# Performance work log

Hardware: AMD Instinct MI355X
Metric: run time of the kernel (lower is better)

Reference implementation:

```python
import jax, jax.numpy as jnp
import numpy as np

L, B, S, D, N, H = 4, 4, 1024, 1024, 64, 16   # layers, batch, seq, d_model, d_state, heads
DI = 2 * D      # d_inner (expand_factor=2)
DH = D // H     # head dim
DF = 4 * D      # ffn hidden
SCALE = 1.0 / np.sqrt(DH)


def setup_inputs() -> dict:
    key = jax.random.key(0)
    ks = jax.random.split(key, 12)
    w = lambda k, sh: jax.random.normal(k, sh, jnp.float32) * 0.02
    return {
        "x": jax.random.normal(ks[0], (B, S, D), jnp.float32),
        "A_log": jax.random.normal(ks[1], (L, N), jnp.float32),
        "Dp": jax.random.normal(ks[2], (L, D), jnp.float32),
        "W_in": w(ks[3], (L, 2 * DI, D)), "b_in": jnp.zeros((L, 2 * DI), jnp.float32),
        "W_xp": w(ks[4], (L, N, DI)), "b_xp": jnp.zeros((L, N), jnp.float32),
        "W_dt": w(ks[5], (L, D, DI)), "b_dt": jnp.zeros((L, D), jnp.float32),
        "W_out": w(ks[6], (L, D, DI)), "b_out": jnp.zeros((L, D), jnp.float32),
        "W_qkv": w(ks[7], (L, 3 * D, D)), "b_qkv": jnp.zeros((L, 3 * D), jnp.float32),
        "W_ao": w(ks[8], (L, D, D)), "b_ao": jnp.zeros((L, D), jnp.float32),
        "g1": jnp.ones((L, D), jnp.float32), "be1": jnp.zeros((L, D), jnp.float32),
        "g2": jnp.ones((L, D), jnp.float32), "be2": jnp.zeros((L, D), jnp.float32),
        "W_f1": w(ks[9], (L, DF, D)), "b_f1": jnp.zeros((L, DF), jnp.float32),
        "W_f2": w(ks[10], (L, D, DF)), "b_f2": jnp.zeros((L, D), jnp.float32),
    }


def _ln(x, g, b, eps=1e-5):
    mu = x.mean(-1, keepdims=True)
    var = ((x - mu) ** 2).mean(-1, keepdims=True)
    return (x - mu) * jax.lax.rsqrt(var + eps) * g + b


def _mamba(x, A_log, Dp, W_in, b_in, W_xp, b_xp, W_dt, b_dt, W_out, b_out):
    xr = jnp.einsum('bsd,od->bso', x, W_in) + b_in          # [b,s,2*DI]
    xi, res = jnp.split(xr, 2, axis=-1)
    xi = jax.nn.silu(xi)
    A = -jnp.exp(A_log)                                      # [N]
    delta = jax.nn.softplus(jnp.einsum('bsi,di->bsd', xi, W_dt) + b_dt)  # [b,s,D]
    m = delta.mean(-1)                                       # [b,s]
    A_disc = jnp.exp(A[None, None, :] * m[:, :, None])       # [b,s,N]
    u = jnp.einsum('bsi,ni->bsn', xi, W_xp) + b_xp           # [b,s,N]

    def step(state, inp):
        a_t, u_t = inp
        state = a_t * state + u_t                            # [b,N]
        return state, state.sum(-1)                          # carry, emit sum over d_state

    init = jnp.zeros((x.shape[0], A_log.shape[0]), x.dtype)
    _, ssum = jax.lax.scan(step, init, (A_disc.swapaxes(0, 1), u.swapaxes(0, 1)))
    ssum = ssum.swapaxes(0, 1)                               # [b,s]
    y = ssum[..., None] * xi                                 # [b,s,DI]
    y = y * jax.nn.silu(res)
    y = jnp.einsum('bsi,di->bsd', y, W_out) + b_out
    return y + x * Dp


def _attn(x, W_qkv, b_qkv, W_ao, b_ao):
    b, s, d = x.shape
    qkv = jnp.einsum('bsd,od->bso', x, W_qkv) + b_qkv        # [b,s,3d]
    qkv = qkv.reshape(b, s, 3, H, DH)
    q = jnp.moveaxis(qkv[:, :, 0], 2, 1)                     # [b,h,s,dh]
    k = jnp.moveaxis(qkv[:, :, 1], 2, 1)
    v = jnp.moveaxis(qkv[:, :, 2], 2, 1)
    scores = jnp.einsum('bhqd,bhkd->bhqk', q, k) * SCALE
    wts = jax.nn.softmax(scores, axis=-1)
    o = jnp.einsum('bhqk,bhkd->bhqd', wts, v)
    o = jnp.moveaxis(o, 1, 2).reshape(b, s, d)
    return jnp.einsum('bsd,od->bso', o, W_ao) + b_ao


def _forward(x, A_log, Dp, W_in, b_in, W_xp, b_xp, W_dt, b_dt, W_out, b_out,
             W_qkv, b_qkv, W_ao, b_ao, g1, be1, g2, be2, W_f1, b_f1, W_f2, b_f2):
    for l in range(L):
        m = _mamba(x, A_log[l], Dp[l], W_in[l], b_in[l], W_xp[l], b_xp[l],
                   W_dt[l], b_dt[l], W_out[l], b_out[l])
        x = _ln(x + m, g1[l], be1[l])
        a = _attn(x, W_qkv[l], b_qkv[l], W_ao[l], b_ao[l])
        x = _ln(x + a, g2[l], be2[l])
        h = jax.nn.gelu(jnp.einsum('bsd,fd->bsf', x, W_f1[l]) + b_f1[l], approximate=False)
        x = x + jnp.einsum('bsf,df->bsd', h, W_f2[l]) + b_f2[l]
    return x


def reference(x, A_log, Dp, W_in, b_in, W_xp, b_xp, W_dt, b_dt, W_out, b_out,
              W_qkv, b_qkv, W_ao, b_ao, g1, be1, g2, be2, W_f1, b_f1, W_f2, b_f2):
    return _forward(x, A_log, Dp, W_in, b_in, W_xp, b_xp, W_dt, b_dt, W_out, b_out,
                    W_qkv, b_qkv, W_ao, b_ao, g1, be1, g2, be2, W_f1, b_f1, W_f2, b_f2)
```

## Files before the change

kernel.cpp:

```cpp
#include <hip/hip_runtime.h>
#include <math.h>

typedef unsigned short ushort_t;
typedef unsigned int uint_t;
typedef __attribute__((ext_vector_type(8))) short short8;
typedef __attribute__((ext_vector_type(4))) float f32x4;

constexpr int Bb = 4, Ss = 1024, Dd = 1024, Nn = 64, Hh = 16;
constexpr int DIi = 2048, DFf = 4096;
constexpr int TOKENS = Bb * Ss;

constexpr size_t O_IN  = 0;
constexpr size_t O_DT  = 4194304;
constexpr size_t O_XP  = O_DT + 2097152;
constexpr size_t O_OUT = O_XP + 262144;
constexpr size_t O_QKV = O_OUT + 2097152;
constexpr size_t O_AO  = O_QKV + 3145728;
constexpr size_t O_F1  = O_AO + 1048576;
constexpr size_t O_F2  = O_F1 + 4194304;
constexpr size_t W_TOTAL = O_F2 + 4194304;
constexpr size_t W_QUADS = W_TOTAL / 4;

enum { EPI_SPLIT = 0, EPI_QKV, EPI_GELU, EPI_DTXP, EPI_DP, EPI_F32, EPI_RESID };

__device__ __forceinline__ float siluf(float x) { return x / (1.f + expf(-x)); }
__device__ __forceinline__ float softplusf(float x) { return fmaxf(x, 0.f) + log1pf(expf(-fabsf(x))); }
__device__ __forceinline__ float geluf(float x) { return 0.5f * x * (1.f + erff(x * 0.7071067811865476f)); }

__device__ __forceinline__ float bf2f(uint_t u) {
    union { uint_t i; float f; } v; v.i = u << 16; return v.f;
}
__device__ __forceinline__ ushort_t f2bf(float f) {
    union { float f; uint_t i; } v; v.f = f;
    return (ushort_t)((v.i + 0x7FFFu + ((v.i >> 16) & 1u)) >> 16);
}

__device__ __forceinline__ void gload_lds16(const ushort_t* g, ushort_t* l) {
    __builtin_amdgcn_global_load_lds(
        (const __attribute__((address_space(1))) unsigned int*)g,
        (__attribute__((address_space(3))) unsigned int*)l, 16, 0, 0);
}

__device__ __forceinline__ void wait_vm(int n) {
    if (n == 0)      asm volatile("s_waitcnt vmcnt(0)" ::: "memory");
    else if (n == 3) asm volatile("s_waitcnt vmcnt(3)" ::: "memory");
    else if (n == 4) asm volatile("s_waitcnt vmcnt(4)" ::: "memory");
    else if (n == 6) asm volatile("s_waitcnt vmcnt(6)" ::: "memory");
    else             asm volatile("s_waitcnt vmcnt(8)" ::: "memory");
}

template <int EPI, int MT, int NBUF, int XBY>
__global__ __launch_bounds__(256) void gemm_mfma(
    const ushort_t* __restrict__ A, const ushort_t* __restrict__ Bw,
    const float* __restrict__ bias, int M, int N, int K,
    float* __restrict__ of0, float* __restrict__ of1,
    ushort_t* __restrict__ ob0, ushort_t* __restrict__ ob1,
    const float* __restrict__ e0, const float* __restrict__ e1)
{
    constexpr int BUFSZ = (MT == 128) ? 8192 : 6144;
    constexpr int DEPTH = NBUF - 1;
    constexpr int L     = (MT == 128) ? 4 : 3;
    constexpr int NJ    = (MT == 128) ? 4 : 2;
    constexpr int XBX   = 8 / XBY;
    __shared__ __attribute__((aligned(16))) ushort_t AB[NBUF * BUFSZ];

    const int tid = threadIdx.x;
    const int lane = tid & 63, wid = tid >> 6;
    const int wr = (MT == 128) ? (wid >> 1) : 0;
    const int wc = (MT == 128) ? (wid & 1) : wid;
    const int l15 = lane & 15, lg = lane >> 4;

    int bx = blockIdx.x, by = blockIdx.y;
    const int gx = gridDim.x, gy = gridDim.y;
    if ((gy % XBY) == 0 && (gx % XBX) == 0) {
        const int s = by * gx + bx;
        const int xcd = s & 7, c = s >> 3;
        const int gyc = gy / XBY, gxc = gx / XBX;
        by = (xcd % XBY) * gyc + (c % gyc);
        bx = (xcd / XBY) * gxc + (c / gyc);
    }
    const int m0 = by * MT, n0 = bx << 7;

    f32x4 acc[4][NJ];
#pragma unroll
    for (int i = 0; i < 4; ++i)
#pragma unroll
        for (int j = 0; j < NJ; ++j) { acc[i][j][0] = 0.f; acc[i][j][1] = 0.f; acc[i][j][2] = 0.f; acc[i][j][3] = 0.f; }

    const int srow4 = lane >> 2;
    const int scc4  = (lane & 3) ^ ((lane >> 3) & 3);
    const ushort_t* Ag = A + (size_t)(m0 + wid * 32 + srow4) * K + scc4 * 8;
    const ushort_t* Bg = Bw + (size_t)(n0 + wid * 32 + srow4) * K + scc4 * 8;
    const ushort_t* sb64[3];
    int do64[3];
    if (MT == 64) {
#pragma unroll
        for (int j = 0; j < 3; ++j) {
            const int i = wid * 3 + j;
            const bool isA = i < 4;
            const int rb = (isA ? i : i - 4) * 16;
            sb64[j] = (isA ? A + (size_t)(m0 + rb + srow4) * K
                           : Bw + (size_t)(n0 + rb + srow4) * K) + scc4 * 8;
            do64[j] = (isA ? 0 : 2048) + rb * 32;
        }
    }

    auto STAGE = [&](int b_, int k0_) {
        ushort_t* d_ = AB + b_ * BUFSZ;
        if constexpr (MT == 128) {
            gload_lds16(Ag + k0_,                  d_ + (wid * 32) * 32);
            gload_lds16(Ag + (size_t)16 * K + k0_, d_ + (wid * 32 + 16) * 32);
            gload_lds16(Bg + k0_,                  d_ + 4096 + (wid * 32) * 32);
            gload_lds16(Bg + (size_t)16 * K + k0_, d_ + 4096 + (wid * 32 + 16) * 32);
        } else {
#pragma unroll
            for (int j = 0; j < 3; ++j)
                gload_lds16(sb64[j] + k0_, d_ + do64[j]);
        }
    };

    const int NS = K >> 5;
#pragma unroll
    for (int p = 0; p < DEPTH; ++p) STAGE(p, p * 32);
    wait_vm((DEPTH - 1) * L);
    __builtin_amdgcn_s_barrier();

    const int chAB = (lg ^ ((l15 >> 1) & 3)) * 8;
    int bc = 0, bp = DEPTH;
    for (int s = 0; s < NS; ++s) {
        if (s + DEPTH < NS) STAGE(bp, (s + DEPTH) << 5);
        const ushort_t* As_ = AB + bc * BUFSZ;
        const ushort_t* Bs_ = As_ + ((MT == 128) ? 4096 : 2048);
        short8 af[4], bfr[NJ];
#pragma unroll
        for (int mi = 0; mi < 4; ++mi)
            af[mi] = *(const short8*)&As_[(wr * 64 + mi * 16 + l15) * 32 + chAB];
#pragma unroll
        for (int nj = 0; nj < NJ; ++nj)
            bfr[nj] = *(const short8*)&Bs_[(wc * (MT == 128 ? 64 : 32) + nj * 16 + l15) * 32 + chAB];
#pragma unroll
        for (int mi = 0; mi < 4; ++mi)
#pragma unroll
            for (int nj = 0; nj < NJ; ++nj)
                acc[mi][nj] = __builtin_amdgcn_mfma_f32_16x16x32_bf16(
                    af[mi], bfr[nj], acc[mi][nj], 0, 0, 0);
        if (s + 1 < NS) {
            const int rem = NS - 2 - s;
            wait_vm(((rem < DEPTH - 1) ? rem : DEPTH - 1) * L);
            __builtin_amdgcn_s_barrier();
        }
        bc = (bc + 1 == NBUF) ? 0 : bc + 1;
        bp = (bp + 1 == NBUF) ? 0 : bp + 1;
    }
    __syncthreads();

    if constexpr (MT == 128) {
        const bool lo = (EPI != EPI_SPLIT) || (n0 < DIi);
#pragma unroll
        for (int nj = 0; nj < 4; ++nj) {
            const int coll = wc * 64 + nj * 16 + l15;
            const float bv = bias[n0 + coll];
#pragma unroll
            for (int mi = 0; mi < 4; ++mi)
#pragma unroll
                for (int r = 0; r < 4; ++r) {
                    float v = acc[mi][nj][r] + bv;
                    if (EPI == EPI_SPLIT) v = lo ? siluf(v) : v;
                    else if (EPI == EPI_GELU) v = geluf(v);
                    AB[(wr * 64 + mi * 16 + lg * 4 + r) * 128 + coll] = f2bf(v);
                }
        }
        __syncthreads();
        if (EPI == EPI_QKV && n0 >= 2048) {
            const int bb = m0 >> 10, srow0 = m0 & 1023;
#pragma unroll
            for (int it = 0; it < 8; ++it) {
                const int task = it * 256 + tid;
                const int dim = task & 127;
                const int strip = task >> 7;
                uint_t w[4];
#pragma unroll
                for (int j = 0; j < 4; ++j) {
                    const int s2 = strip * 8 + 2 * j;
                    w[j] = (uint_t)AB[s2 * 128 + dim] | ((uint_t)AB[(s2 + 1) * 128 + dim] << 16);
                }
                const int vd = (n0 - 2048) + dim;
                *(uint4*)&ob1[((size_t)(bb * Hh + (vd >> 6)) * 64 + (vd & 63)) * Ss + srow0 + strip * 8] =
                    make_uint4(w[0], w[1], w[2], w[3]);
            }
        } else {
            ushort_t* dst = (EPI == EPI_SPLIT) ? (lo ? ob0 : ob1) : ob0;
            const int Nd = (EPI == EPI_SPLIT) ? DIi : N;
            const int nb = (EPI == EPI_SPLIT && !lo) ? (n0 - DIi) : n0;
#pragma unroll
            for (int i = 0; i < 8; ++i) {
                const int c = i * 256 + tid;
                const int row = c >> 4, ch = c & 15;
                *(uint4*)&dst[(size_t)(m0 + row) * Nd + nb + ch * 8] =
                    *(const uint4*)&AB[row * 128 + ch * 8];
            }
        }
    } else {
        float* Cf = (float*)AB;
#pragma unroll
        for (int nj = 0; nj < NJ; ++nj) {
            const int coll = wc * 32 + nj * 16 + l15;
            const float bv = bias[n0 + coll];
#pragma unroll
            for (int mi = 0; mi < 4; ++mi)
#pragma unroll
                for (int r = 0; r < 4; ++r)
                    Cf[(mi * 16 + lg * 4 + r) * 128 + coll] = acc[mi][nj][r] + bv;
        }
        __syncthreads();
#pragma unroll
        for (int i = 0; i < 8; ++i) {
            const int c = i * 256 + tid;
            const int row = c >> 5, ch = c & 31;
            const int grow = m0 + row;
            const int gcol = n0 + ch * 4;
            float4 v = *(const float4*)&Cf[row * 128 + ch * 4];
            if (EPI == EPI_DTXP) {
                if (n0 < Dd) {
                    float ps = softplusf(v.x) + softplusf(v.y) + softplusf(v.z) + softplusf(v.w);
#pragma unroll
                    for (int off = 1; off < 32; off <<= 1) ps += __shfl_xor(ps, off);
                    if ((lane & 31) == 0)
                        of0[(size_t)grow * 8 + (n0 >> 7)] = ps;
                } else {
                    *(float4*)&of1[(size_t)grow * 128 + (gcol - Dd)] = v;
                }
            } else if (EPI == EPI_DP) {
                const float4 e = *(const float4*)&e0[(size_t)grow * N + gcol];
                const float4 d = *(const float4*)&e1[gcol];
                v.x = fmaf(e.x, d.x, v.x); v.y = fmaf(e.y, d.y, v.y);
                v.z = fmaf(e.z, d.z, v.z); v.w = fmaf(e.w, d.w, v.w);
                *(float4*)&of0[(size_t)grow * N + gcol] = v;
            } else if (EPI == EPI_F32) {
                *(float4*)&of0[(size_t)grow * N + gcol] = v;
            } else {
                const float4 e = *(const float4*)&e0[(size_t)grow * N + gcol];
                v.x += e.x; v.y += e.y; v.z += e.z; v.w += e.w;
                *(float4*)&of0[(size_t)grow * N + gcol] = v;
                uint2 w;
                w.x = (uint_t)f2bf(v.x) | ((uint_t)f2bf(v.y) << 16);
                w.y = (uint_t)f2bf(v.z) | ((uint_t)f2bf(v.w) << 16);
                *(uint2*)&ob0[(size_t)grow * N + gcol] = w;
            }
        }
    }
}

__global__ __launch_bounds__(256) void convert_weights_kernel(
    const float* __restrict__ Win, const float* __restrict__ Wdt,
    const float* __restrict__ Wxp, const float* __restrict__ Wout,
    const float* __restrict__ Wqkv, const float* __restrict__ Wao,
    const float* __restrict__ Wf1, const float* __restrict__ Wf2,
    const float* __restrict__ bdt, const float* __restrict__ bxp,
    ushort_t* __restrict__ dst, float* __restrict__ bcat)
{
    size_t q = (size_t)blockIdx.x * blockDim.x + threadIdx.x;
    if (q < 288) {
#pragma unroll
        for (int j = 0; j < 4; ++j) {
            const int e = (int)q * 4 + j;
            bcat[e] = (e < Dd) ? bdt[e] : ((e < Dd + Nn) ? bxp[e - Dd] : 0.f);
        }
    }
    const size_t stride = (size_t)gridDim.x * blockDim.x;
    for (; q < W_QUADS; q += stride) {
        const size_t e = q * 4;
        float4 v;
        if (e < O_DT)       v = *(const float4*)&Win[e - O_IN];
        else if (e < O_XP)  v = *(const float4*)&Wdt[e - O_DT];
        else if (e < O_OUT) {
            const size_t li = e - O_XP;
            const int row = (int)(li >> 11), colq = (int)(li & 2047);
            v = (row < Nn) ? *(const float4*)&Wxp[(size_t)row * DIi + colq]
                           : make_float4(0.f, 0.f, 0.f, 0.f);
        }
        else if (e < O_QKV) v = *(const float4*)&Wout[e - O_OUT];
        else if (e < O_AO)  v = *(const float4*)&Wqkv[e - O_QKV];
        else if (e < O_F1)  v = *(const float4*)&Wao[e - O_AO];
        else if (e < O_F2)  v = *(const float4*)&Wf1[e - O_F1];
        else                v = *(const float4*)&Wf2[e - O_F2];
        uint2 w;
        w.x = (uint_t)f2bf(v.x) | ((uint_t)f2bf(v.y) << 16);
        w.y = (uint_t)f2bf(v.z) | ((uint_t)f2bf(v.w) << 16);
        *(uint2*)&dst[e] = w;
    }
}

__global__ __launch_bounds__(256) void cvt_f32_bf16_kernel(
    const float* __restrict__ in, ushort_t* __restrict__ out)
{
    const size_t i4 = (size_t)blockIdx.x * blockDim.x + threadIdx.x;
    const float4 v = *(const float4*)&in[i4 * 4];
    uint2 w;
    w.x = (uint_t)f2bf(v.x) | ((uint_t)f2bf(v.y) << 16);
    w.y = (uint_t)f2bf(v.z) | ((uint_t)f2bf(v.w) << 16);
    *(uint2*)&out[i4 * 4] = w;
}

__global__ __launch_bounds__(256) void ln_residual_kernel(
    float* __restrict__ xio, const float* __restrict__ addin,
    const float* __restrict__ g, const float* __restrict__ be,
    ushort_t* __restrict__ xb)
{
    __shared__ float red[8];
    const int tid = threadIdx.x;
    const size_t base = (size_t)blockIdx.x * Dd;
    const float4 xv = *(const float4*)&xio[base + tid * 4];
    const float4 av = *(const float4*)&addin[base + tid * 4];
    float v[4] = {xv.x + av.x, xv.y + av.y, xv.z + av.z, xv.w + av.w};
    float s = v[0] + v[1] + v[2] + v[3];
    float s2 = v[0] * v[0] + v[1] * v[1] + v[2] * v[2] + v[3] * v[3];
#pragma unroll
    for (int off = 32; off; off >>= 1) { s += __shfl_xor(s, off); s2 += __shfl_xor(s2, off); }
    if ((tid & 63) == 0) { red[tid >> 6] = s; red[4 + (tid >> 6)] = s2; }
    __syncthreads();
    const float mu = (red[0] + red[1] + red[2] + red[3]) * (1.f / (float)Dd);
    const float var = (red[4] + red[5] + red[6] + red[7]) * (1.f / (float)Dd) - mu * mu;
    const float rstd = rsqrtf(var + 1e-5f);
    const float4 gv = *(const float4*)&g[tid * 4];
    const float4 bv = *(const float4*)&be[tid * 4];
    float o[4];
    o[0] = (v[0] - mu) * rstd * gv.x + bv.x;
    o[1] = (v[1] - mu) * rstd * gv.y + bv.y;
    o[2] = (v[2] - mu) * rstd * gv.z + bv.z;
    o[3] = (v[3] - mu) * rstd * gv.w + bv.w;
    *(float4*)&xio[base + tid * 4] = make_float4(o[0], o[1], o[2], o[3]);
    uint2 w;
    w.x = (uint_t)f2bf(o[0]) | ((uint_t)f2bf(o[1]) << 16);
    w.y = (uint_t)f2bf(o[2]) | ((uint_t)f2bf(o[3]) << 16);
    *(uint2*)&xb[base + tid * 4] = w;
}

__global__ __launch_bounds__(1024) void scan_fused_kernel(
    const float* __restrict__ A_log_l, const float* __restrict__ part,
    const float* __restrict__ u, float* __restrict__ ssum)
{
    __shared__ float Ps[16][64];
    __shared__ float Sl[16][64];
    __shared__ float Cs[16][64];
    __shared__ float Ms[16][64];
    const int b = blockIdx.x;
    const int tid = threadIdx.x;
    const int n = tid & 63, c = tid >> 6;
    const int t0 = b * Ss + c * 64;
    const float Aval = -expf(A_log_l[n]);

    {
        const float* pp = part + (size_t)(t0 + n) * 8;
        float ps = 0.f;
#pragma unroll
        for (int j = 0; j < 8; ++j) ps += pp[j];
        Ms[c][n] = ps * (1.f / 1024.f);
    }
    __syncthreads();

    float S = 0.f, msum = 0.f;
#pragma unroll 8
    for (int t = 0; t < 64; ++t) {
        const float mt = Ms[c][t];
        msum += mt;
        S = fmaf(expf(Aval * mt), S, u[(size_t)(t0 + t) * 128 + n]);
    }
    Ps[c][n] = expf(Aval * msum);
    Sl[c][n] = S;
    __syncthreads();

    if (c == 0) {
        float carry = 0.f;
#pragma unroll
        for (int cc = 0; cc < 16; ++cc) {
            Cs[cc][n] = carry;
            carry = fmaf(Ps[cc][n], carry, Sl[cc][n]);
        }
    }
    __syncthreads();

    float st = Cs[c][n];
#pragma unroll 4
    for (int t = 0; t < 64; ++t) {
        st = fmaf(expf(Aval * Ms[c][t]), st, u[(size_t)(t0 + t) * 128 + n]);
        float r = st;
#pragma unroll
        for (int off = 32; off; off >>= 1) r += __shfl_xor(r, off);
        if (n == 0) ssum[t0 + t] = r;
    }
}

__global__ __launch_bounds__(256) void y_gate_kernel(
    ushort_t* __restrict__ xi, const ushort_t* __restrict__ res,
    const float* __restrict__ ssum)
{
    const size_t i8 = (size_t)blockIdx.x * blockDim.x + threadIdx.x;
    const int t = (int)(i8 >> 8);
    const float sv = ssum[t];
    uint4 xw = *(const uint4*)&xi[i8 * 8];
    const uint4 rw = *(const uint4*)&res[i8 * 8];
    const uint_t xs[4] = {xw.x, xw.y, xw.z, xw.w};
    const uint_t rs[4] = {rw.x, rw.y, rw.z, rw.w};
    uint_t os[4];
#pragma unroll
    for (int j = 0; j < 4; ++j) {
        const float x0 = bf2f(xs[j] & 0xffffu), x1 = bf2f(xs[j] >> 16);
        const float r0 = bf2f(rs[j] & 0xffffu), r1 = bf2f(rs[j] >> 16);
        os[j] = (uint_t)f2bf(sv * x0 * siluf(r0)) | ((uint_t)f2bf(sv * x1 * siluf(r1)) << 16);
    }
    *(uint4*)&xi[i8 * 8] = make_uint4(os[0], os[1], os[2], os[3]);
}

__global__ __launch_bounds__(256) void attn_mfma_kernel(
    const ushort_t* __restrict__ qkv, const ushort_t* __restrict__ vt,
    ushort_t* __restrict__ out)
{
    __shared__ ushort_t Ks[64 * 64];
    __shared__ ushort_t Vs[64 * 64];
    __shared__ __attribute__((aligned(16))) ushort_t Pb[4][2560];

    const int tid = threadIdx.x;
    const int lane = tid & 63, wid = tid >> 6;
    const int b = blockIdx.z, h = blockIdx.y;
    const int q0 = blockIdx.x * 128 + wid * 32;
    const int l15 = lane & 15, lg = lane >> 4;
    constexpr float CEXP = 0.125f * 1.44269504f;

    short8 qf[2][2];
#pragma unroll
    for (int mi = 0; mi < 2; ++mi)
#pragma unroll
        for (int kk = 0; kk < 2; ++kk)
            qf[mi][kk] = *(const short8*)&qkv[(size_t)(b * Ss + q0 + mi * 16 + l15) * 3072
                                              + h * 64 + kk * 32 + lg * 8];

    f32x4 oacc[2][4];
#pragma unroll
    for (int mi = 0; mi < 2; ++mi)
#pragma unroll
        for (int nj = 0; nj < 4; ++nj) { oacc[mi][nj][0]=0.f; oacc[mi][nj][1]=0.f; oacc[mi][nj][2]=0.f; oacc[mi][nj][3]=0.f; }
    float lrun[2][4];
#pragma unroll
    for (int mi = 0; mi < 2; ++mi)
#pragma unroll
        for (int r = 0; r < 4; ++r) lrun[mi][r] = 0.f;

    const int srow = lane >> 3;
    const int scc  = (lane & 7) ^ srow;
    const ushort_t* Kg = qkv + (size_t)(b * Ss + wid * 16 + srow) * 3072 + 1024 + h * 64 + scc * 8;
    const ushort_t* Vg = vt + (size_t)((b * Hh + h) * 64 + wid * 16 + srow) * Ss + scc * 8;

    for (int kt = 0; kt < Ss / 64; ++kt) {
#pragma unroll
        for (int j = 0; j < 2; ++j) {
            gload_lds16(Kg + (size_t)(kt * 64 + j * 8) * 3072, Ks + (wid * 16 + j * 8) * 64);
            gload_lds16(Vg + (size_t)j * 8 * Ss + kt * 64,     Vs + (wid * 16 + j * 8) * 64);
        }
        __syncthreads();

        f32x4 sacc[2][4];
#pragma unroll
        for (int mi = 0; mi < 2; ++mi)
#pragma unroll
            for (int nj = 0; nj < 4; ++nj) { sacc[mi][nj][0]=0.f; sacc[mi][nj][1]=0.f; sacc[mi][nj][2]=0.f; sacc[mi][nj][3]=0.f; }
#pragma unroll
        for (int kk = 0; kk < 2; ++kk) {
            short8 kf[4];
#pragma unroll
            for (int nj = 0; nj < 4; ++nj) {
                const int row = nj * 16 + l15;
                const int ch = (kk * 4 + lg) ^ (row & 7);
                kf[nj] = *(const short8*)&Ks[row * 64 + ch * 8];
            }
#pragma unroll
            for (int mi = 0; mi < 2; ++mi)
#pragma unroll
                for (int nj = 0; nj < 4; ++nj)
                    sacc[mi][nj] = __builtin_amdgcn_mfma_f32_16x16x32_bf16(
                        qf[mi][kk], kf[nj], sacc[mi][nj], 0, 0, 0);
        }

#pragma unroll
        for (int mi = 0; mi < 2; ++mi)
#pragma unroll
            for (int nj = 0; nj < 4; ++nj) {
                const int bi = mi * 2 + (nj >> 1);
                const int chsw = ((nj & 1) * 2 + (l15 >> 3)) ^ lg;
#pragma unroll
                for (int r = 0; r < 4; ++r) {
                    const float p = exp2f(sacc[mi][nj][r] * CEXP);
                    lrun[mi][r] += p;
                    const int q15 = lg * 4 + r;
                    Pb[wid][bi * 640 + q15 * 40 + chsw * 8 + (lane & 7)] = f2bf(p);
                }
            }

#pragma unroll
        for (int kk = 0; kk < 2; ++kk) {
            short8 pa[2], vb[4];
#pragma unroll
            for (int mi = 0; mi < 2; ++mi) {
                const int chsw = lg ^ (l15 >> 2);
                pa[mi] = *(const short8*)&Pb[wid][(mi * 2 + kk) * 640 + l15 * 40 + chsw * 8];
            }
#pragma unroll
            for (int nj = 0; nj < 4; ++nj) {
                const int row = nj * 16 + l15;
                const int ch = (kk * 4 + lg) ^ (row & 7);
                vb[nj] = *(const short8*)&Vs[row * 64 + ch * 8];
            }
#pragma unroll
            for (int mi = 0; mi < 2; ++mi)
#pragma unroll
                for (int nj = 0; nj < 4; ++nj)
                    oacc[mi][nj] = __builtin_amdgcn_mfma_f32_16x16x32_bf16(
                        pa[mi], vb[nj], oacc[mi][nj], 0, 0, 0);
        }
        __syncthreads();
    }

#pragma unroll
    for (int mi = 0; mi < 2; ++mi)
#pragma unroll
        for (int r = 0; r < 4; ++r) {
            float s = lrun[mi][r];
#pragma unroll
            for (int off = 1; off < 16; off <<= 1) s += __shfl_xor(s, off);
            lrun[mi][r] = 1.f / s;
        }
#pragma unroll
    for (int mi = 0; mi < 2; ++mi)
#pragma unroll
        for (int r = 0; r < 4; ++r) {
            const int q = q0 + mi * 16 + lg * 4 + r;
            const float inv = lrun[mi][r];
#pragma unroll
            for (int nj = 0; nj < 4; ++nj)
                out[(size_t)(b * Ss + q) * Dd + h * 64 + nj * 16 + l15] =
                    f2bf(oacc[mi][nj][r] * inv);
        }
}

extern "C" void kernel_launch(void* const* d_in, const int* in_sizes, int n_in,
                              void* d_out, int out_size, void* d_ws, size_t ws_size,
                              hipStream_t stream)
{
    const float* x_in  = (const float*)d_in[0];
    const float* A_log = (const float*)d_in[1];
    const float* Dp    = (const float*)d_in[2];
    const float* W_in  = (const float*)d_in[3];
    const float* b_in  = (const float*)d_in[4];
    const float* W_xp  = (const float*)d_in[5];
    const float* b_xp  = (const float*)d_in[6];
    const float* W_dt  = (const float*)d_in[7];
    const float* b_dt  = (const float*)d_in[8];
    const float* W_out = (const float*)d_in[9];
    const float* b_out = (const float*)d_in[10];
    const float* W_qkv = (const float*)d_in[11];
    const float* b_qkv = (const float*)d_in[12];
    const float* W_ao  = (const float*)d_in[13];
    const float* b_ao  = (const float*)d_in[14];
    const float* g1    = (const float*)d_in[15];
    const float* be1   = (const float*)d_in[16];
    const float* g2    = (const float*)d_in[17];
    const float* be2   = (const float*)d_in[18];
    const float* W_f1  = (const float*)d_in[19];
    const float* b_f1  = (const float*)d_in[20];
    const float* W_f2  = (const float*)d_in[21];
    const float* b_f2  = (const float*)d_in[22];

    float* xf      = (float*)d_ws;
    float* a3      = xf + 4194304;
    float* ub      = a3 + 4194304;
    float* sb      = ub + 524288;
    float* part    = sb + 4096;
    float* bcat    = part + 32768;
    ushort_t* xb    = (ushort_t*)(bcat + 1152);
    ushort_t* xi_b  = xb + 4194304;
    ushort_t* res_b = xi_b + 8388608;
    ushort_t* qh_b  = res_b + 8388608;
    ushort_t* ao_b  = qh_b + 16777216;
    ushort_t* Wb    = ao_b + 4194304;
    ushort_t* vt_b  = Wb + W_TOTAL;

    hipMemcpyAsync(xf, x_in, (size_t)TOKENS * Dd * sizeof(float),
                   hipMemcpyDeviceToDevice, stream);
    cvt_f32_bf16_kernel<<<dim3(4096), dim3(256), 0, stream>>>(x_in, xb);

    const dim3 blk(256);

    for (int l = 0; l < 4; ++l) {
        convert_weights_kernel<<<dim3(2048), blk, 0, stream>>>(
            W_in + (size_t)l * 4194304, W_dt + (size_t)l * 2097152,
            W_xp + (size_t)l * 131072,  W_out + (size_t)l * 2097152,
            W_qkv + (size_t)l * 3145728, W_ao + (size_t)l * 1048576,
            W_f1 + (size_t)l * 4194304, W_f2 + (size_t)l * 4194304,
            b_dt + (size_t)l * 1024, b_xp + (size_t)l * Nn, Wb, bcat);

        gemm_mfma<EPI_SPLIT, 128, 4, 4><<<dim3(32, 32), blk, 0, stream>>>(
            xb, Wb + O_IN, b_in + (size_t)l * 4096, TOKENS, 4096, 1024,
            nullptr, nullptr, xi_b, res_b, nullptr, nullptr);
        gemm_mfma<EPI_DTXP, 64, 4, 8><<<dim3(9, 64), blk, 0, stream>>>(
            xi_b, Wb + O_DT, bcat, TOKENS, 1152, 2048,
            part, ub, nullptr, nullptr, nullptr, nullptr);
        scan_fused_kernel<<<dim3(Bb), dim3(1024), 0, stream>>>(
            A_log + (size_t)l * Nn, part, ub, sb);
        y_gate_kernel<<<dim3(4096), blk, 0, stream>>>(xi_b, res_b, sb);
        gemm_mfma<EPI_DP, 64, 4, 8><<<dim3(8, 64), blk, 0, stream>>>(
            xi_b, Wb + O_OUT, b_out + (size_t)l * 1024, TOKENS, 1024, 2048,
            a3, nullptr, nullptr, nullptr, xf, Dp + (size_t)l * 1024);
        ln_residual_kernel<<<dim3(TOKENS), blk, 0, stream>>>(
            xf, a3, g1 + (size_t)l * 1024, be1 + (size_t)l * 1024, xb);
        gemm_mfma<EPI_QKV, 128, 3, 4><<<dim3(24, 32), blk, 0, stream>>>(
            xb, Wb + O_QKV, b_qkv + (size_t)l * 3072, TOKENS, 3072, 1024,
            nullptr, nullptr, qh_b, vt_b, nullptr, nullptr);
        attn_mfma_kernel<<<dim3(8, Hh, Bb), blk, 0, stream>>>(qh_b, vt_b, ao_b);
        gemm_mfma<EPI_F32, 64, 4, 8><<<dim3(8, 64), blk, 0, stream>>>(
            ao_b, Wb + O_AO, b_ao + (size_t)l * 1024, TOKENS, 1024, 1024,
            a3, nullptr, nullptr, nullptr, nullptr, nullptr);
        ln_residual_kernel<<<dim3(TOKENS), blk, 0, stream>>>(
            xf, a3, g2 + (size_t)l * 1024, be2 + (size_t)l * 1024, xb);
        gemm_mfma<EPI_GELU, 128, 4, 4><<<dim3(32, 32), blk, 0, stream>>>(
            xb, Wb + O_F1, b_f1 + (size_t)l * 4096, TOKENS, 4096, 1024,
            nullptr, nullptr, qh_b, nullptr, nullptr, nullptr);
        gemm_mfma<EPI_RESID, 64, 4, 8><<<dim3(8, 64), blk, 0, stream>>>(
            qh_b, Wb + O_F2, b_f2 + (size_t)l * 1024, TOKENS, 1024, 4096,
            xf, nullptr, xb, nullptr, xf, nullptr);
    }

    hipMemcpyAsync(d_out, xf, (size_t)TOKENS * Dd * sizeof(float),
                   hipMemcpyDeviceToDevice, stream);
    (void)in_sizes; (void)n_in; (void)out_size; (void)ws_size;
}
```

Before: 1.819 ms.

## Add 256x256-tile 512-thread GEMM for wide-N projections

```diff
diff --git a/kernel.cpp b/kernel.cpp
--- a/kernel.cpp
+++ b/kernel.cpp
@@ -49,80 +49,55 @@
     else             asm volatile("s_waitcnt vmcnt(8)" ::: "memory");
 }
 
-template <int EPI, int MT, int NBUF, int XBY>
-__global__ __launch_bounds__(256) void gemm_mfma(
+template <int EPI>
+__global__ __launch_bounds__(512) void gemm_mfma256(
     const ushort_t* __restrict__ A, const ushort_t* __restrict__ Bw,
     const float* __restrict__ bias, int M, int N, int K,
-    float* __restrict__ of0, float* __restrict__ of1,
-    ushort_t* __restrict__ ob0, ushort_t* __restrict__ ob1,
-    const float* __restrict__ e0, const float* __restrict__ e1)
-{
-    constexpr int BUFSZ = (MT == 128) ? 8192 : 6144;
-    constexpr int DEPTH = NBUF - 1;
-    constexpr int L     = (MT == 128) ? 4 : 3;
-    constexpr int NJ    = (MT == 128) ? 4 : 2;
-    constexpr int XBX   = 8 / XBY;
+    ushort_t* __restrict__ ob0, ushort_t* __restrict__ ob1)
+{
+    constexpr int NBUF = 3, DEPTH = 2, L = 4;
+    constexpr int BUFSZ = 16384;
     __shared__ __attribute__((aligned(16))) ushort_t AB[NBUF * BUFSZ];
 
     const int tid = threadIdx.x;
     const int lane = tid & 63, wid = tid >> 6;
-    const int wr = (MT == 128) ? (wid >> 1) : 0;
-    const int wc = (MT == 128) ? (wid & 1) : wid;
+    const int wr = wid >> 2, wc = wid & 3;
     const int l15 = lane & 15, lg = lane >> 4;
 
     int bx = blockIdx.x, by = blockIdx.y;
     const int gx = gridDim.x, gy = gridDim.y;
-    if ((gy % XBY) == 0 && (gx % XBX) == 0) {
+    if ((gy & 3) == 0 && (gx & 1) == 0) {
         const int s = by * gx + bx;
         const int xcd = s & 7, c = s >> 3;
-        const int gyc = gy / XBY, gxc = gx / XBX;
-        by = (xcd % XBY) * gyc + (c % gyc);
-        bx = (xcd / XBY) * gxc + (c / gyc);
-    }
-    const int m0 = by * MT, n0 = bx << 7;
-
-    f32x4 acc[4][NJ];
-#pragma unroll
-    for (int i = 0; i < 4; ++i)
-#pragma unroll
-        for (int j = 0; j < NJ; ++j) { acc[i][j][0] = 0.f; acc[i][j][1] = 0.f; acc[i][j][2] = 0.f; acc[i][j][3] = 0.f; }
+        const int gyc = gy >> 2, gxc = gx >> 1;
+        by = (xcd & 3) * gyc + (c % gyc);
+        bx = (xcd >> 2) * gxc + (c / gyc);
+    }
+    const int m0 = by << 8, n0 = bx << 8;
+
+    f32x4 acc[8][4];
+#pragma unroll
+    for (int i = 0; i < 8; ++i)
+#pragma unroll
+        for (int j = 0; j < 4; ++j) { acc[i][j][0]=0.f; acc[i][j][1]=0.f; acc[i][j][2]=0.f; acc[i][j][3]=0.f; }
 
     const int srow4 = lane >> 2;
     const int scc4  = (lane & 3) ^ ((lane >> 3) & 3);
     const ushort_t* Ag = A + (size_t)(m0 + wid * 32 + srow4) * K + scc4 * 8;
     const ushort_t* Bg = Bw + (size_t)(n0 + wid * 32 + srow4) * K + scc4 * 8;
-    const ushort_t* sb64[3];
-    int do64[3];
-    if (MT == 64) {
-#pragma unroll
-        for (int j = 0; j < 3; ++j) {
-            const int i = wid * 3 + j;
-            const bool isA = i < 4;
-            const int rb = (isA ? i : i - 4) * 16;
-            sb64[j] = (isA ? A + (size_t)(m0 + rb + srow4) * K
-                           : Bw + (size_t)(n0 + rb + srow4) * K) + scc4 * 8;
-            do64[j] = (isA ? 0 : 2048) + rb * 32;
-        }
-    }
 
     auto STAGE = [&](int b_, int k0_) {
         ushort_t* d_ = AB + b_ * BUFSZ;
-        if constexpr (MT == 128) {
-            gload_lds16(Ag + k0_,                  d_ + (wid * 32) * 32);
-            gload_lds16(Ag + (size_t)16 * K + k0_, d_ + (wid * 32 + 16) * 32);
-            gload_lds16(Bg + k0_,                  d_ + 4096 + (wid * 32) * 32);
-            gload_lds16(Bg + (size_t)16 * K + k0_, d_ + 4096 + (wid * 32 + 16) * 32);
-        } else {
-#pragma unroll
-            for (int j = 0; j < 3; ++j)
-                gload_lds16(sb64[j] + k0_, d_ + do64[j]);
-        }
+        gload_lds16(Ag + k0_,                  d_ + (wid * 32) * 32);
+        gload_lds16(Ag + (size_t)16 * K + k0_, d_ + (wid * 32 + 16) * 32);
+        gload_lds16(Bg + k0_,                  d_ + 8192 + (wid * 32) * 32);
+        gload_lds16(Bg + (size_t)16 * K + k0_, d_ + 8192 + (wid * 32 + 16) * 32);
     };
 
     const int NS = K >> 5;
-#pragma unroll
-    for (int p = 0; p < DEPTH; ++p) STAGE(p, p * 32);
-    wait_vm((DEPTH - 1) * L);
+    STAGE(0, 0);
+    STAGE(1, 32);
+    wait_vm(4);
     __builtin_amdgcn_s_barrier();
 
     const int chAB = (lg ^ ((l15 >> 1) & 3)) * 8;
@@ -130,23 +105,22 @@
     for (int s = 0; s < NS; ++s) {
         if (s + DEPTH < NS) STAGE(bp, (s + DEPTH) << 5);
         const ushort_t* As_ = AB + bc * BUFSZ;
-        const ushort_t* Bs_ = As_ + ((MT == 128) ? 4096 : 2048);
-        short8 af[4], bfr[NJ];
-#pragma unroll
-        for (int mi = 0; mi < 4; ++mi)
-            af[mi] = *(const short8*)&As_[(wr * 64 + mi * 16 + l15) * 32 + chAB];
-#pragma unroll
-        for (int nj = 0; nj < NJ; ++nj)
-            bfr[nj] = *(const short8*)&Bs_[(wc * (MT == 128 ? 64 : 32) + nj * 16 + l15) * 32 + chAB];
-#pragma unroll
-        for (int mi = 0; mi < 4; ++mi)
-#pragma unroll
-            for (int nj = 0; nj < NJ; ++nj)
+        const ushort_t* Bs_ = As_ + 8192;
+        short8 af[8], bfr[4];
+#pragma unroll
+        for (int mi = 0; mi < 8; ++mi)
+            af[mi] = *(const short8*)&As_[(wr * 128 + mi * 16 + l15) * 32 + chAB];
+#pragma unroll
+        for (int nj = 0; nj < 4; ++nj)
+            bfr[nj] = *(const short8*)&Bs_[(wc * 64 + nj * 16 + l15) * 32 + chAB];
+#pragma unroll
+        for (int mi = 0; mi < 8; ++mi)
+#pragma unroll
+            for (int nj = 0; nj < 4; ++nj)
                 acc[mi][nj] = __builtin_amdgcn_mfma_f32_16x16x32_bf16(
                     af[mi], bfr[nj], acc[mi][nj], 0, 0, 0);
         if (s + 1 < NS) {
-            const int rem = NS - 2 - s;
-            wait_vm(((rem < DEPTH - 1) ? rem : DEPTH - 1) * L);
+            wait_vm((s + 2 < NS) ? 4 : 0);
             __builtin_amdgcn_s_barrier();
         }
         bc = (bc + 1 == NBUF) ? 0 : bc + 1;
@@ -154,35 +128,40 @@
     }
     __syncthreads();
 
-    if constexpr (MT == 128) {
-        const bool lo = (EPI != EPI_SPLIT) || (n0 < DIi);
-#pragma unroll
-        for (int nj = 0; nj < 4; ++nj) {
-            const int coll = wc * 64 + nj * 16 + l15;
-            const float bv = bias[n0 + coll];
-#pragma unroll
-            for (int mi = 0; mi < 4; ++mi)
-#pragma unroll
-                for (int r = 0; r < 4; ++r) {
-                    float v = acc[mi][nj][r] + bv;
-                    if (EPI == EPI_SPLIT) v = lo ? siluf(v) : v;
-                    else if (EPI == EPI_GELU) v = geluf(v);
-                    AB[(wr * 64 + mi * 16 + lg * 4 + r) * 128 + coll] = f2bf(v);
-                }
+    const bool lo = (EPI != EPI_SPLIT) || (n0 < DIi);
+#pragma unroll
+    for (int pass = 0; pass < 2; ++pass) {
+        if (pass) __syncthreads();
+        if (wr == pass) {
+#pragma unroll
+            for (int nj = 0; nj < 4; ++nj) {
+                const int coll = wc * 64 + nj * 16 + l15;
+                const float bv = bias[n0 + coll];
+#pragma unroll
+                for (int mi = 0; mi < 8; ++mi)
+#pragma unroll
+                    for (int r = 0; r < 4; ++r) {
+                        float v = acc[mi][nj][r] + bv;
+                        if (EPI == EPI_SPLIT) v = lo ? siluf(v) : v;
+                        else if (EPI == EPI_GELU) v = geluf(v);
+                        AB[(mi * 16 + lg * 4 + r) * 256 + coll] = f2bf(v);
+                    }
+            }
         }
         __syncthreads();
+        const int tok0 = m0 + pass * 128;
         if (EPI == EPI_QKV && n0 >= 2048) {
-            const int bb = m0 >> 10, srow0 = m0 & 1023;
+            const int bb = tok0 >> 10, srow0 = tok0 & 1023;
 #pragma unroll
             for (int it = 0; it < 8; ++it) {
-                const int task = it * 256 + tid;
-                const int dim = task & 127;
-                const int strip = task >> 7;
+                const int task = it * 512 + tid;
+                const int dim = task & 255;
+                const int strip = task >> 8;
                 uint_t w[4];
 #pragma unroll
                 for (int j = 0; j < 4; ++j) {
                     const int s2 = strip * 8 + 2 * j;
-                    w[j] = (uint_t)AB[s2 * 128 + dim] | ((uint_t)AB[(s2 + 1) * 128 + dim] << 16);
+                    w[j] = (uint_t)AB[s2 * 256 + dim] | ((uint_t)AB[(s2 + 1) * 256 + dim] << 16);
                 }
                 const int vd = (n0 - 2048) + dim;
                 *(uint4*)&ob1[((size_t)(bb * Hh + (vd >> 6)) * 64 + (vd & 63)) * Ss + srow0 + strip * 8] =
@@ -193,12 +172,140 @@
             const int Nd = (EPI == EPI_SPLIT) ? DIi : N;
             const int nb = (EPI == EPI_SPLIT && !lo) ? (n0 - DIi) : n0;
 #pragma unroll
-            for (int i = 0; i < 8; ++i) {
-                const int c = i * 256 + tid;
-                const int row = c >> 4, ch = c & 15;
-                *(uint4*)&dst[(size_t)(m0 + row) * Nd + nb + ch * 8] =
-                    *(const uint4*)&AB[row * 128 + ch * 8];
+            for (int it = 0; it < 8; ++it) {
+                const int c = it * 512 + tid;
+                const int row = c >> 5, ch = c & 31;
+                *(uint4*)&dst[(size_t)(tok0 + row) * Nd + nb + ch * 8] =
+                    *(const uint4*)&AB[row * 256 + ch * 8];
             }
+        }
+    }
+}
+
+template <int EPI, int MT, int NBUF, int XBY>
+__global__ __launch_bounds__(256) void gemm_mfma(
+    const ushort_t* __restrict__ A, const ushort_t* __restrict__ Bw,
+    const float* __restrict__ bias, int M, int N, int K,
+    float* __restrict__ of0, float* __restrict__ of1,
+    ushort_t* __restrict__ ob0, ushort_t* __restrict__ ob1,
+    const float* __restrict__ e0, const float* __restrict__ e1)
+{
+    constexpr int BUFSZ = (MT == 128) ? 8192 : 6144;
+    constexpr int DEPTH = NBUF - 1;
+    constexpr int L     = (MT == 128) ? 4 : 3;
+    constexpr int NJ    = (MT == 128) ? 4 : 2;
+    constexpr int XBX   = 8 / XBY;
+    __shared__ __attribute__((aligned(16))) ushort_t AB[NBUF * BUFSZ];
+
+    const int tid = threadIdx.x;
+    const int lane = tid & 63, wid = tid >> 6;
+    const int wr = (MT == 128) ? (wid >> 1) : 0;
+    const int wc = (MT == 128) ? (wid & 1) : wid;
+    const int l15 = lane & 15, lg = lane >> 4;
+
+    int bx = blockIdx.x, by = blockIdx.y;
+    const int gx = gridDim.x, gy = gridDim.y;
+    if ((gy % XBY) == 0 && (gx % XBX) == 0) {
+        const int s = by * gx + bx;
+        const int xcd = s & 7, c = s >> 3;
+        const int gyc = gy / XBY, gxc = gx / XBX;
+        by = (xcd % XBY) * gyc + (c % gyc);
+        bx = (xcd / XBY) * gxc + (c / gyc);
+    }
+    const int m0 = by * MT, n0 = bx << 7;
+
+    f32x4 acc[4][NJ];
+#pragma unroll
+    for (int i = 0; i < 4; ++i)
+#pragma unroll
+        for (int j = 0; j < NJ; ++j) { acc[i][j][0] = 0.f; acc[i][j][1] = 0.f; acc[i][j][2] = 0.f; acc[i][j][3] = 0.f; }
+
+    const int srow4 = lane >> 2;
+    const int scc4  = (lane & 3) ^ ((lane >> 3) & 3);
+    const ushort_t* Ag = A + (size_t)(m0 + wid * 32 + srow4) * K + scc4 * 8;
+    const ushort_t* Bg = Bw + (size_t)(n0 + wid * 32 + srow4) * K + scc4 * 8;
+    const ushort_t* sb64[3];
+    int do64[3];
+    if (MT == 64) {
+#pragma unroll
+        for (int j = 0; j < 3; ++j) {
+            const int i = wid * 3 + j;
+            const bool isA = i < 4;
+            const int rb = (isA ? i : i - 4) * 16;
+            sb64[j] = (isA ? A + (size_t)(m0 + rb + srow4) * K
+                           : Bw + (size_t)(n0 + rb + srow4) * K) + scc4 * 8;
+            do64[j] = (isA ? 0 : 2048) + rb * 32;
+        }
+    }
+
+    auto STAGE = [&](int b_, int k0_) {
+        ushort_t* d_ = AB + b_ * BUFSZ;
+        if constexpr (MT == 128) {
+            gload_lds16(Ag + k0_,                  d_ + (wid * 32) * 32);
+            gload_lds16(Ag + (size_t)16 * K + k0_, d_ + (wid * 32 + 16) * 32);
+            gload_lds16(Bg + k0_,                  d_ + 4096 + (wid * 32) * 32);
+            gload_lds16(Bg + (size_t)16 * K + k0_, d_ + 4096 + (wid * 32 + 16) * 32);
+        } else {
+#pragma unroll
+            for (int j = 0; j < 3; ++j)
+                gload_lds16(sb64[j] + k0_, d_ + do64[j]);
+        }
+    };
+
+    const int NS = K >> 5;
+#pragma unroll
+    for (int p = 0; p < DEPTH; ++p) STAGE(p, p * 32);
+    wait_vm((DEPTH - 1) * L);
+    __builtin_amdgcn_s_barrier();
+
+    const int chAB = (lg ^ ((l15 >> 1) & 3)) * 8;
+    int bc = 0, bp = DEPTH;
+    for (int s = 0; s < NS; ++s) {
+        if (s + DEPTH < NS) STAGE(bp, (s + DEPTH) << 5);
+        const ushort_t* As_ = AB + bc * BUFSZ;
+        const ushort_t* Bs_ = As_ + ((MT == 128) ? 4096 : 2048);
+        short8 af[4], bfr[NJ];
+#pragma unroll
+        for (int mi = 0; mi < 4; ++mi)
+            af[mi] = *(const short8*)&As_[(wr * 64 + mi * 16 + l15) * 32 + chAB];
+#pragma unroll
+        for (int nj = 0; nj < NJ; ++nj)
+            bfr[nj] = *(const short8*)&Bs_[(wc * (MT == 128 ? 64 : 32) + nj * 16 + l15) * 32 + chAB];
+#pragma unroll
+        for (int mi = 0; mi < 4; ++mi)
+#pragma unroll
+            for (int nj = 0; nj < NJ; ++nj)
+                acc[mi][nj] = __builtin_amdgcn_mfma_f32_16x16x32_bf16(
+                    af[mi], bfr[nj], acc[mi][nj], 0, 0, 0);
+        if (s + 1 < NS) {
+            const int rem = NS - 2 - s;
+            wait_vm(((rem < DEPTH - 1) ? rem : DEPTH - 1) * L);
+            __builtin_amdgcn_s_barrier();
+        }
+        bc = (bc + 1 == NBUF) ? 0 : bc + 1;
+        bp = (bp + 1 == NBUF) ? 0 : bp + 1;
+    }
+    __syncthreads();
+
+    if constexpr (MT == 128) {
+        const bool lo = true; (void)lo;
+#pragma unroll
+        for (int nj = 0; nj < 4; ++nj) {
+            const int coll = wc * 64 + nj * 16 + l15;
+            const float bv = bias[n0 + coll];
+#pragma unroll
+            for (int mi = 0; mi < 4; ++mi)
+#pragma unroll
+                for (int r = 0; r < 4; ++r)
+                    AB[(wr * 64 + mi * 16 + lg * 4 + r) * 128 + coll] = f2bf(acc[mi][nj][r] + bv);
+        }
+        __syncthreads();
+#pragma unroll
+        for (int i = 0; i < 8; ++i) {
+            const int c = i * 256 + tid;
+            const int row = c >> 4, ch = c & 15;
+            *(uint4*)&ob0[(size_t)(m0 + row) * N + n0 + ch * 8] =
+                *(const uint4*)&AB[row * 128 + ch * 8];
         }
     } else {
         float* Cf = (float*)AB;
@@ -588,7 +695,7 @@
                    hipMemcpyDeviceToDevice, stream);
     cvt_f32_bf16_kernel<<<dim3(4096), dim3(256), 0, stream>>>(x_in, xb);
 
-    const dim3 blk(256);
+    const dim3 blk(256), blk512(512);
 
     for (int l = 0; l < 4; ++l) {
         convert_weights_kernel<<<dim3(2048), blk, 0, stream>>>(
@@ -598,9 +705,9 @@
             W_f1 + (size_t)l * 4194304, W_f2 + (size_t)l * 4194304,
             b_dt + (size_t)l * 1024, b_xp + (size_t)l * Nn, Wb, bcat);
 
-        gemm_mfma<EPI_SPLIT, 128, 4, 4><<<dim3(32, 32), blk, 0, stream>>>(
+        gemm_mfma256<EPI_SPLIT><<<dim3(16, 16), blk512, 0, stream>>>(
             xb, Wb + O_IN, b_in + (size_t)l * 4096, TOKENS, 4096, 1024,
-            nullptr, nullptr, xi_b, res_b, nullptr, nullptr);
+            xi_b, res_b);
         gemm_mfma<EPI_DTXP, 64, 4, 8><<<dim3(9, 64), blk, 0, stream>>>(
             xi_b, Wb + O_DT, bcat, TOKENS, 1152, 2048,
             part, ub, nullptr, nullptr, nullptr, nullptr);
@@ -612,18 +719,18 @@
             a3, nullptr, nullptr, nullptr, xf, Dp + (size_t)l * 1024);
         ln_residual_kernel<<<dim3(TOKENS), blk, 0, stream>>>(
             xf, a3, g1 + (size_t)l * 1024, be1 + (size_t)l * 1024, xb);
-        gemm_mfma<EPI_QKV, 128, 3, 4><<<dim3(24, 32), blk, 0, stream>>>(
+        gemm_mfma256<EPI_QKV><<<dim3(12, 16), blk512, 0, stream>>>(
             xb, Wb + O_QKV, b_qkv + (size_t)l * 3072, TOKENS, 3072, 1024,
-            nullptr, nullptr, qh_b, vt_b, nullptr, nullptr);
+            qh_b, vt_b);
         attn_mfma_kernel<<<dim3(8, Hh, Bb), blk, 0, stream>>>(qh_b, vt_b, ao_b);
         gemm_mfma<EPI_F32, 64, 4, 8><<<dim3(8, 64), blk, 0, stream>>>(
             ao_b, Wb + O_AO, b_ao + (size_t)l * 1024, TOKENS, 1024, 1024,
             a3, nullptr, nullptr, nullptr, nullptr, nullptr);
         ln_residual_kernel<<<dim3(TOKENS), blk, 0, stream>>>(
             xf, a3, g2 + (size_t)l * 1024, be2 + (size_t)l * 1024, xb);
-        gemm_mfma<EPI_GELU, 128, 4, 4><<<dim3(32, 32), blk, 0, stream>>>(
+        gemm_mfma256<EPI_GELU><<<dim3(16, 16), blk512, 0, stream>>>(
             xb, Wb + O_F1, b_f1 + (size_t)l * 4096, TOKENS, 4096, 1024,
-            nullptr, nullptr, qh_b, nullptr, nullptr, nullptr);
+            qh_b, nullptr);
         gemm_mfma<EPI_RESID, 64, 4, 8><<<dim3(8, 64), blk, 0, stream>>>(
             qh_b, Wb + O_F2, b_f2 + (size_t)l * 1024, TOKENS, 1024, 4096,
             xf, nullptr, xb, nullptr, xf, nullptr);
```

Result: slower. 1.864 ms (+2.5%).
